# Kernel tuning notes

Measured on AMD Instinct MI355X. Metric: run time of the kernel, lower is better.

The kernel has to match this reference:

```python
import jax, jax.numpy as jnp
import numpy as np

GN_EPS = 1e-5
NN_EPS = 1e-8


def _three_nn_interpolate(xyz1, xyz2, points2):
    # xyz1: (B,N,3), xyz2: (B,M,3), points2: (B,M,C) -> (B,N,C)
    src_sq = jnp.sum(xyz1 ** 2, axis=-1, keepdims=True)          # (B,N,1)
    dst_sq = jnp.sum(xyz2 ** 2, axis=-1)[:, None, :]             # (B,1,M)
    inner = jnp.einsum('bnd,bmd->bnm', xyz1, xyz2)               # (B,N,M)
    dist = src_sq - 2.0 * inner + dst_sq                         # (B,N,M)
    neg_d, idx = jax.lax.top_k(-dist, 3)                         # (B,N,3)
    d = -neg_d
    inv = 1.0 / (d + NN_EPS)
    w = inv / jnp.sum(inv, axis=-1, keepdims=True)               # (B,N,3)
    grouped = jax.vmap(lambda p, i: p[i])(points2, idx)          # (B,N,3,C)
    return jnp.sum(grouped * w[..., None], axis=2)               # (B,N,C)


def _group_norm(x, weight, bias, groups):
    # x: (B,C,N)
    B, C, N = x.shape
    xg = x.reshape(B, groups, C // groups, N)
    mu = jnp.mean(xg, axis=(2, 3), keepdims=True)
    var = jnp.var(xg, axis=(2, 3), keepdims=True)
    xg = (xg - mu) * jax.lax.rsqrt(var + GN_EPS)
    x = xg.reshape(B, C, N)
    return x * weight[None, :, None] + bias[None, :, None]


def setup_inputs() -> dict:
    key = jax.random.key(0)
    ks = jax.random.split(key, 10)
    B, N, M, C1, C2 = 8, 8192, 2048, 128, 256
    mlp = [256, 128]
    in_ch = C1 + C2
    inp = {
        'xyz1': jax.random.normal(ks[0], (B, N, 3), dtype=jnp.float32),
        'xyz2': jax.random.normal(ks[1], (B, M, 3), dtype=jnp.float32),
        'points1': jax.random.normal(ks[2], (B, N, C1), dtype=jnp.float32),
        'points2': jax.random.normal(ks[3], (B, M, C2), dtype=jnp.float32),
        'w0': jax.random.normal(ks[4], (mlp[0], in_ch), dtype=jnp.float32) * (1.0 / np.sqrt(in_ch)),
        'w1': jax.random.normal(ks[5], (mlp[1], mlp[0]), dtype=jnp.float32) * (1.0 / np.sqrt(mlp[0])),
        'gn0_w': jnp.ones((mlp[0],), dtype=jnp.float32),
        'gn0_b': jnp.zeros((mlp[0],), dtype=jnp.float32),
        'gn1_w': jnp.ones((mlp[1],), dtype=jnp.float32),
        'gn1_b': jnp.zeros((mlp[1],), dtype=jnp.float32),
    }
    return inp


def reference(xyz1, xyz2, points1, points2, w0, w1, gn0_w, gn0_b, gn1_w, gn1_b):
    interpolated = _three_nn_interpolate(xyz1, xyz2, points2)    # (B,N,C2)
    feat = jnp.concatenate([points1, interpolated], axis=-1)     # (B,N,C1+C2)
    # conv1d kernel size 1 == pointwise matmul; work in (B,C,N) layout for GN
    h = jnp.einsum('bnc,oc->bon', feat, w0)                      # (B,256,N)
    h = jax.nn.relu(_group_norm(h, gn0_w, gn0_b, groups=min(32, w0.shape[0])))
    h = jnp.einsum('bcn,oc->bon', h, w1)                         # (B,128,N)
    h = jax.nn.relu(_group_norm(h, gn1_w, gn1_b, groups=min(32, w1.shape[0])))
    return jnp.transpose(h, (0, 2, 1))                           # (B,N,128)
```

## Files before the change

### kernel.cpp

```cpp
#include <hip/hip_runtime.h>


#define DEVI __device__ __forceinline__

static constexpr int B  = 8;
static constexpr int N  = 8192;
static constexpr int M  = 2048;
static constexpr int C1 = 128;
static constexpr int C2 = 256;
static constexpr int CIN = C1 + C2;
static constexpr int H0 = 256;
static constexpr int H1 = 128;
static constexpr int BN = B * N;
static constexpr int NSEG = 8;
static constexpr int SEGL = M / NSEG;
static constexpr int SL = 64;

typedef __bf16 bf16x8 __attribute__((ext_vector_type(8)));
typedef float  f32x4  __attribute__((ext_vector_type(4)));
typedef unsigned short ushort8v __attribute__((ext_vector_type(8)));

DEVI float bf2f(unsigned short u) {
    union { unsigned int i; float f; } v; v.i = ((unsigned int)u) << 16; return v.f;
}
DEVI unsigned short f2bf(float f) {
    union { float f; unsigned int i; } v; v.f = f;
    unsigned int x = v.i;
    return (unsigned short)((x + 0x7fffu + ((x >> 16) & 1u)) >> 16);
}
DEVI float ldin(const void* p, size_t i, int bf) {
    return bf ? bf2f(((const unsigned short*)p)[i]) : ((const float*)p)[i];
}
DEVI void ld8(const void* p, size_t i, int bf, float r[8]) {
    if (bf) {
        const ushort8v u = *(const ushort8v*)((const unsigned short*)p + i);
#pragma unroll
        for (int k = 0; k < 8; k++) r[k] = bf2f(u[k]);
    } else {
        const float4 a = *(const float4*)((const float*)p + i);
        const float4 b = *(const float4*)((const float*)p + i + 4);
        r[0] = a.x; r[1] = a.y; r[2] = a.z; r[3] = a.w;
        r[4] = b.x; r[5] = b.y; r[6] = b.z; r[7] = b.w;
    }
}

DEVI void gload16(const void* g, void* l) {
    __builtin_amdgcn_global_load_lds(
        (const __attribute__((address_space(1))) void*)g,
        (__attribute__((address_space(3))) void*)l, 16, 0, 0);
}

__global__ __launch_bounds__(64) void detect_dtype_kernel(const void* __restrict__ xyz1,
                                                          int* __restrict__ flag)
{
    const unsigned short* u = (const unsigned short*)xyz1;
    const int lane = threadIdx.x;
    const float av = fabsf(bf2f(u[2 * lane]));
    const bool in_range = (av >= 1e-4f && av <= 100.0f);
    const unsigned long long m = __ballot(in_range);
    if (lane == 0) flag[0] = (__popcll(m) >= 32) ? 1 : 0;
}

__global__ __launch_bounds__(256) void prep_kernel(
    const void* __restrict__ w0, const void* __restrict__ w1,
    const void* __restrict__ xyz2,
    unsigned short* __restrict__ w0b, unsigned short* __restrict__ w1b,
    float4* __restrict__ c4, const int* __restrict__ flag)
{
    const int bf = flag[0];
    const int n0 = H0 * CIN;
    const int n1 = H1 * H0;
    const int n2 = B * M;
    const int total = n0 + n1 + n2;
    for (int i = blockIdx.x * blockDim.x + threadIdx.x; i < total; i += gridDim.x * blockDim.x) {
        if (i < n0) {
            w0b[i] = bf ? ((const unsigned short*)w0)[i] : f2bf(((const float*)w0)[i]);
        } else if (i < n0 + n1) {
            const int j = i - n0;
            w1b[j] = bf ? ((const unsigned short*)w1)[j] : f2bf(((const float*)w1)[j]);
        } else {
            const int j = i - n0 - n1;
            const float x = ldin(xyz2, (size_t)j * 3 + 0, bf);
            const float y = ldin(xyz2, (size_t)j * 3 + 1, bf);
            const float z = ldin(xyz2, (size_t)j * 3 + 2, bf);
            const float sq = __fadd_rn(__fadd_rn(__fmul_rn(x, x), __fmul_rn(y, y)), __fmul_rn(z, z));
            c4[j] = make_float4(x, y, z, 0.5f * sq);
        }
    }
}

__global__ __launch_bounds__(256) void knn3_split_kernel(
    const void* __restrict__ xyz1, const float4* __restrict__ c4,
    int* __restrict__ ci, const int* __restrict__ flag)
{
    const int bf = flag[0];
    const int tid = threadIdx.x;
    const int gid = blockIdx.x * 256 + tid;
    const int s = blockIdx.y;
    const int b = __builtin_amdgcn_readfirstlane(gid >> 13);

    const float x1 = ldin(xyz1, (size_t)gid * 3 + 0, bf);
    const float y1 = ldin(xyz1, (size_t)gid * 3 + 1, bf);
    const float z1 = ldin(xyz1, (size_t)gid * 3 + 2, bf);

    const float4* __restrict__ cand = c4 + b * M + s * SEGL;
    const int jbase = s * SEGL;

    float b0 = 3.4e38f, b1 = 3.4e38f, b2 = 3.4e38f;
    int   i0 = 0, i1 = 0, i2 = 0;

#pragma unroll 4
    for (int j = 0; j < SEGL; ++j) {
        const float4 p = cand[j];
        const float sc = __builtin_fmaf(-x1, p.x,
                          __builtin_fmaf(-y1, p.y,
                           __builtin_fmaf(-z1, p.z, p.w)));
        const int jn = jbase + j;
        const bool c0 = sc < b0;
        const float t1 = fmaxf(sc, b0);
        b0 = fminf(sc, b0);
        const int  tj1 = c0 ? i0 : jn;
        i0 = c0 ? jn : i0;
        const bool c1 = t1 < b1;
        const float t2 = fmaxf(t1, b1);
        b1 = fminf(t1, b1);
        const int  tj2 = c1 ? i1 : tj1;
        i1 = c1 ? tj1 : i1;
        const bool c2 = t2 < b2;
        b2 = fminf(t2, b2);
        i2 = c2 ? tj2 : i2;
    }

    ci[(size_t)(s * 3 + 0) * BN + gid] = i0;
    ci[(size_t)(s * 3 + 1) * BN + gid] = i1;
    ci[(size_t)(s * 3 + 2) * BN + gid] = i2;
}

__global__ __launch_bounds__(256) void knn3_merge_kernel(
    const void* __restrict__ xyz1, const float4* __restrict__ c4,
    const int* __restrict__ ci,
    int* __restrict__ nn_idx, float* __restrict__ nn_w,
    const int* __restrict__ flag)
{
    const int bf = flag[0];
    const int gid = blockIdx.x * 256 + threadIdx.x;
    const int b = gid >> 13;

    const float x1 = ldin(xyz1, (size_t)gid * 3 + 0, bf);
    const float y1 = ldin(xyz1, (size_t)gid * 3 + 1, bf);
    const float z1 = ldin(xyz1, (size_t)gid * 3 + 2, bf);
    const float sq1 = __fadd_rn(__fadd_rn(__fmul_rn(x1, x1), __fmul_rn(y1, y1)), __fmul_rn(z1, z1));

    float bd0 = 3.4e38f, bd1 = 3.4e38f, bd2 = 3.4e38f;
    int   bi0 = 0x7fffffff, bi1 = 0x7fffffff, bi2 = 0x7fffffff;

#pragma unroll
    for (int k = 0; k < 3 * NSEG; ++k) {
        const int ix = ci[(size_t)k * BN + gid];
        const float4 p = c4[b * M + ix];
        const float inner = __fadd_rn(__fadd_rn(__fmul_rn(x1, p.x), __fmul_rn(y1, p.y)),
                                      __fmul_rn(z1, p.z));
        const float pw2 = p.w + p.w;
        const float d = __fadd_rn(__fsub_rn(sq1, __fmul_rn(2.0f, inner)), pw2);
        const bool lt2 = (d < bd2) || (d == bd2 && ix < bi2);
        if (lt2) {
            const bool lt0 = (d < bd0) || (d == bd0 && ix < bi0);
            const bool lt1 = (d < bd1) || (d == bd1 && ix < bi1);
            if (lt0)      { bd2 = bd1; bi2 = bi1; bd1 = bd0; bi1 = bi0; bd0 = d; bi0 = ix; }
            else if (lt1) { bd2 = bd1; bi2 = bi1; bd1 = d; bi1 = ix; }
            else          { bd2 = d; bi2 = ix; }
        }
    }

    const float v0 = 1.0f / (bd0 + 1e-8f);
    const float v1 = 1.0f / (bd1 + 1e-8f);
    const float v2 = 1.0f / (bd2 + 1e-8f);
    const float s = v0 + v1 + v2;
    nn_idx[gid * 3 + 0] = bi0; nn_idx[gid * 3 + 1] = bi1; nn_idx[gid * 3 + 2] = bi2;
    nn_w[gid * 3 + 0] = v0 / s; nn_w[gid * 3 + 1] = v1 / s; nn_w[gid * 3 + 2] = v2 / s;
}

__global__ __launch_bounds__(256) void interp_concat_kernel(
    const void* __restrict__ p1, const void* __restrict__ p2,
    const int* __restrict__ nn_idx, const float* __restrict__ nn_w,
    unsigned short* __restrict__ feat, const int* __restrict__ flag)
{
    const int bf = flag[0];
    const int total = BN * (CIN / 8);
    for (int idx = blockIdx.x * blockDim.x + threadIdx.x; idx < total; idx += gridDim.x * blockDim.x) {
        const int c8 = idx % 48;
        const int p  = idx / 48;
        const int c  = c8 * 8;
        float r[8];
        if (c < C1) {
            ld8(p1, (size_t)p * C1 + c, bf, r);
        } else {
            const int b  = p >> 13;
            const int c2 = c - C1;
            const int*   id = nn_idx + p * 3;
            const float* wv = nn_w  + p * 3;
            float t0[8], t1[8], t2[8];
            ld8(p2, (size_t)(b * M + id[0]) * C2 + c2, bf, t0);
            ld8(p2, (size_t)(b * M + id[1]) * C2 + c2, bf, t1);
            ld8(p2, (size_t)(b * M + id[2]) * C2 + c2, bf, t2);
            const float w0v = wv[0], w1v = wv[1], w2v = wv[2];
#pragma unroll
            for (int k = 0; k < 8; k++) r[k] = w0v * t0[k] + w1v * t1[k] + w2v * t2[k];
        }
        ushort8v o;
#pragma unroll
        for (int k = 0; k < 8; k++) o[k] = f2bf(r[k]);
        *(ushort8v*)(feat + (size_t)idx * 8) = o;
    }
}

template<int K, int COUT>
__global__ __launch_bounds__(256) void gemm_mfma_kernel(
    const unsigned short* __restrict__ A,
    const unsigned short* __restrict__ W,
    unsigned short* __restrict__ Cmat)
{
    __shared__ __align__(16) char lds[32768];

    const int tid = threadIdx.x;
    const int l   = tid & 63;
    const int w   = tid >> 6;
    const int rowBase = blockIdx.x * 128;
    const int colBase = blockIdx.y * 128;

    const int srow  = l >> 3;
    const int sslot = l & 7;

    f32x4 acc[4][4];
#pragma unroll
    for (int i = 0; i < 4; i++)
#pragma unroll
        for (int j = 0; j < 4; j++) acc[i][j] = (f32x4)0.0f;

    const int wr  = (tid >> 7) & 1;
    const int wc  = (tid >> 6) & 1;
    const int rl  = l & 15;
    const int kq  = l >> 4;
    const int swz = (l & 7) << 4;
    int aoff[4], boff[4];
#pragma unroll
    for (int i = 0; i < 4; i++) {
        aoff[i] = (wr * 64 + i * 16 + rl) * 128;
        boff[i] = 16384 + (wc * 64 + i * 16 + rl) * 128;
    }

    constexpr int NT = K / 64;

#pragma unroll 1
    for (int t = 0; t < NT; ++t) {
        {
            const int k0 = t * 64;
#pragma unroll
            for (int i = 0; i < 4; ++i) {
                const int ch = w * 4 + i;
                const int r  = ch * 8 + srow;
                const int ke = (sslot ^ (r & 7)) << 3;
                gload16(A + ((size_t)(rowBase + r) * K + k0 + ke), lds + ch * 1024);
                gload16(W + ((size_t)(colBase + r) * K + k0 + ke), lds + 16384 + ch * 1024);
            }
        }
        __syncthreads();
#pragma unroll
        for (int ks = 0; ks < 2; ++ks) {
            const int kb = (ks * 64 + kq * 16) ^ swz;
            bf16x8 af[4], bfr[4];
#pragma unroll
            for (int i = 0; i < 4; i++) af[i]  = *(const bf16x8*)(lds + aoff[i] + kb);
#pragma unroll
            for (int j = 0; j < 4; j++) bfr[j] = *(const bf16x8*)(lds + boff[j] + kb);
#pragma unroll
            for (int i = 0; i < 4; i++)
#pragma unroll
                for (int j = 0; j < 4; j++)
                    acc[i][j] = __builtin_amdgcn_mfma_f32_16x16x32_bf16(af[i], bfr[j], acc[i][j], 0, 0, 0);
        }
        __syncthreads();
    }

    const int crow = rowBase + wr * 64 + kq * 4;
    const int ccol = colBase + wc * 64 + rl;
#pragma unroll
    for (int i = 0; i < 4; i++)
#pragma unroll
        for (int j = 0; j < 4; j++)
#pragma unroll
            for (int r = 0; r < 4; r++)
                Cmat[(size_t)(crow + i * 16 + r) * COUT + ccol + j * 16] = f2bf(acc[i][j][r]);
}

__global__ __launch_bounds__(256) void gn_stats_part_kernel(
    const unsigned short* __restrict__ h, float2* __restrict__ part, int C)
{
    const int cpg = C >> 5;
    const int b  = blockIdx.x / SL;
    const int sl = blockIdx.x % SL;
    const int g  = threadIdx.x & 31;
    const int rs = threadIdx.x >> 5;
    const int rows = N / SL;

    float s = 0.f, ss = 0.f;
    for (int n = sl * rows + rs; n < (sl + 1) * rows; n += 8) {
        const unsigned short* row = h + (size_t)(b * N + n) * C + g * cpg;
        for (int c = 0; c < cpg; c += 4) {
            const ushort4 v = *(const ushort4*)(row + c);
            const float f0 = bf2f(v.x), f1 = bf2f(v.y), f2 = bf2f(v.z), f3 = bf2f(v.w);
            s  += f0 + f1 + f2 + f3;
            ss += f0 * f0 + f1 * f1 + f2 * f2 + f3 * f3;
        }
    }
    __shared__ float2 red[256];
    red[threadIdx.x] = make_float2(s, ss);
    __syncthreads();
    if (threadIdx.x < 32) {
        float2 a = red[threadIdx.x];
#pragma unroll
        for (int k = 1; k < 8; k++) {
            const float2 p = red[threadIdx.x + 32 * k];
            a.x += p.x; a.y += p.y;
        }
        part[(size_t)blockIdx.x * 32 + g] = a;
    }
}

__global__ __launch_bounds__(256) void gn_finalize_kernel(
    const float2* __restrict__ part, float2* __restrict__ st, int C)
{
    const int t = threadIdx.x;
    const int b = t >> 5;
    const int g = t & 31;
    const int cpg = C >> 5;
    float s = 0.f, ss = 0.f;
    for (int k = 0; k < SL; k++) {
        const float2 p = part[(size_t)(b * SL + k) * 32 + g];
        s += p.x; ss += p.y;
    }
    const float cnt = (float)N * (float)cpg;
    const float mu  = s / cnt;
    const float var = ss / cnt - mu * mu;
    st[t] = make_float2(mu, rsqrtf(var + 1e-5f));
}

__global__ __launch_bounds__(256) void gn_norm_relu_kernel(
    const unsigned short* __restrict__ h, const float2* __restrict__ st,
    const void* __restrict__ gw, const void* __restrict__ gb,
    void* __restrict__ out, int C, int cpg, int total4,
    const int* __restrict__ flag, int final_out)
{
    const int bf = flag[0];
    const int C4 = C >> 2;
    for (int i4 = blockIdx.x * blockDim.x + threadIdx.x; i4 < total4; i4 += gridDim.x * blockDim.x) {
        const int c = (i4 % C4) * 4;
        const int p = i4 / C4;
        const int b = p >> 13;
        const float2 ms = st[b * (C / cpg) + c / cpg];
        const ushort4 hv = *(const ushort4*)(h + (size_t)i4 * 4);
        float r[4] = { bf2f(hv.x), bf2f(hv.y), bf2f(hv.z), bf2f(hv.w) };
#pragma unroll
        for (int k = 0; k < 4; k++) {
            const float gwv = ldin(gw, c + k, bf);
            const float gbv = ldin(gb, c + k, bf);
            r[k] = fmaxf((r[k] - ms.x) * ms.y * gwv + gbv, 0.f);
        }
        if (!final_out || bf) {
            ushort4 o;
            o.x = f2bf(r[0]); o.y = f2bf(r[1]); o.z = f2bf(r[2]); o.w = f2bf(r[3]);
            *(ushort4*)((unsigned short*)out + (size_t)i4 * 4) = o;
        } else {
            float4 o; o.x = r[0]; o.y = r[1]; o.z = r[2]; o.w = r[3];
            *(float4*)((float*)out + (size_t)i4 * 4) = o;
        }
    }
}

extern "C" void kernel_launch(void* const* d_in, const int* in_sizes, int n_in,
                              void* d_out, int out_size, void* d_ws, size_t ws_size,
                              hipStream_t stream)
{
    const void* xyz1    = d_in[0];
    const void* xyz2    = d_in[1];
    const void* points1 = d_in[2];
    const void* points2 = d_in[3];
    const void* w0      = d_in[4];
    const void* w1      = d_in[5];
    const void* gn0w    = d_in[6];
    const void* gn0b    = d_in[7];
    const void* gn1w    = d_in[8];
    const void* gn1b    = d_in[9];

    char* ws = (char*)d_ws;
    int*            nn_idx = (int*)ws;
    float*          nn_w   = (float*)(ws + 786432);
    unsigned short* feat   = (unsigned short*)(ws + 1572864);
    unsigned short* h0     = (unsigned short*)(ws + 51904512);
    unsigned short* h0n    = feat;
    unsigned short* h1     = h0;
    unsigned short* w0b    = (unsigned short*)(ws + 85458944);
    unsigned short* w1b    = (unsigned short*)(ws + 85655552);
    float2*         st0    = (float2*)(ws + 85721088);
    float2*         st1    = (float2*)(ws + 85723136);
    int*            flag   = (int*)(ws + 85725184);
    float4*         c4     = (float4*)(ws + 85725248);
    int*            ci     = (int*)(ws + 85987392);
    float2*         part   = (float2*)(ws + 92278848);

    detect_dtype_kernel<<<1, 64, 0, stream>>>(xyz1, flag);

    prep_kernel<<<576, 256, 0, stream>>>(w0, w1, xyz2, w0b, w1b, c4, flag);

    {
        dim3 g(BN / 256, NSEG);
        knn3_split_kernel<<<g, 256, 0, stream>>>(xyz1, c4, ci, flag);
    }
    knn3_merge_kernel<<<BN / 256, 256, 0, stream>>>(xyz1, c4, ci, nn_idx, nn_w, flag);

    interp_concat_kernel<<<2048, 256, 0, stream>>>(points1, points2, nn_idx, nn_w, feat, flag);

    {
        dim3 g(BN / 128, H0 / 128);
        gemm_mfma_kernel<CIN, H0><<<g, 256, 0, stream>>>(feat, w0b, h0);
    }

    gn_stats_part_kernel<<<B * SL, 256, 0, stream>>>(h0, part, H0);
    gn_finalize_kernel<<<1, 256, 0, stream>>>(part, st0, H0);
    gn_norm_relu_kernel<<<2048, 256, 0, stream>>>(h0, st0, gn0w, gn0b, (void*)h0n,
                                                  H0, H0 / 32, BN * H0 / 4, flag, 0);

    {
        dim3 g(BN / 128, H1 / 128);
        gemm_mfma_kernel<H0, H1><<<g, 256, 0, stream>>>(h0n, w1b, h1);
    }

    gn_stats_part_kernel<<<B * SL, 256, 0, stream>>>(h1, part, H1);
    gn_finalize_kernel<<<1, 256, 0, stream>>>(part, st1, H1);
    gn_norm_relu_kernel<<<1024, 256, 0, stream>>>(h1, st1, gn1w, gn1b, d_out,
                                                  H1, H1 / 32, BN * H1 / 4, flag, 1);
}
```

Before: 331.7 us.

## Fuse interpolation into GEMM1, GN0 normalize into GEMM2, and GN stats into epilogues

Interpolation and concat now happen while staging the A tile of the first GEMM, so the feat buffer is never written or read back. GroupNorm0 normalize+ReLU is applied while loading the second GEMM's A tile, and GroupNorm statistics are accumulated in the GEMM epilogues with LDS and global atomics. This drops several separate kernels and full-tensor passes. It also splits the KNN scan into two independent interleaved top-3 chains for more ILP. The costs are gather latency inside the GEMM loop, a larger LDS footprint, and float atomics that make the statistics order nondeterministic.

```diff
diff --git a/kernel.cpp b/kernel.cpp
--- a/kernel.cpp
+++ b/kernel.cpp
@@ -14,7 +14,6 @@
 static constexpr int BN = B * N;
 static constexpr int NSEG = 8;
 static constexpr int SEGL = M / NSEG;
-static constexpr int SL = 64;
 
 typedef __bf16 bf16x8 __attribute__((ext_vector_type(8)));
 typedef float  f32x4  __attribute__((ext_vector_type(4)));
@@ -65,26 +64,30 @@
     const void* __restrict__ w0, const void* __restrict__ w1,
     const void* __restrict__ xyz2,
     unsigned short* __restrict__ w0b, unsigned short* __restrict__ w1b,
-    float4* __restrict__ c4, const int* __restrict__ flag)
+    float4* __restrict__ c4, float* __restrict__ partz,
+    const int* __restrict__ flag)
 {
     const int bf = flag[0];
     const int n0 = H0 * CIN;
     const int n1 = H1 * H0;
     const int n2 = B * M;
-    const int total = n0 + n1 + n2;
+    const int n3 = 1024;
+    const int total = n0 + n1 + n2 + n3;
     for (int i = blockIdx.x * blockDim.x + threadIdx.x; i < total; i += gridDim.x * blockDim.x) {
         if (i < n0) {
             w0b[i] = bf ? ((const unsigned short*)w0)[i] : f2bf(((const float*)w0)[i]);
         } else if (i < n0 + n1) {
             const int j = i - n0;
             w1b[j] = bf ? ((const unsigned short*)w1)[j] : f2bf(((const float*)w1)[j]);
-        } else {
+        } else if (i < n0 + n1 + n2) {
             const int j = i - n0 - n1;
             const float x = ldin(xyz2, (size_t)j * 3 + 0, bf);
             const float y = ldin(xyz2, (size_t)j * 3 + 1, bf);
             const float z = ldin(xyz2, (size_t)j * 3 + 2, bf);
             const float sq = __fadd_rn(__fadd_rn(__fmul_rn(x, x), __fmul_rn(y, y)), __fmul_rn(z, z));
             c4[j] = make_float4(x, y, z, 0.5f * sq);
+        } else {
+            partz[i - n0 - n1 - n2] = 0.f;
         }
     }
 }
@@ -105,35 +108,65 @@
 
     const float4* __restrict__ cand = c4 + b * M + s * SEGL;
     const int jbase = s * SEGL;
-
-    float b0 = 3.4e38f, b1 = 3.4e38f, b2 = 3.4e38f;
-    int   i0 = 0, i1 = 0, i2 = 0;
+    constexpr int HALF = SEGL / 2;
+
+    float a0 = 3.4e38f, a1 = 3.4e38f, a2 = 3.4e38f;
+    int   ia0 = 0, ia1 = 0, ia2 = 0;
+    float g0 = 3.4e38f, g1 = 3.4e38f, g2 = 3.4e38f;
+    int   ig0 = 0, ig1 = 0, ig2 = 0;
 
 #pragma unroll 4
-    for (int j = 0; j < SEGL; ++j) {
-        const float4 p = cand[j];
-        const float sc = __builtin_fmaf(-x1, p.x,
-                          __builtin_fmaf(-y1, p.y,
-                           __builtin_fmaf(-z1, p.z, p.w)));
-        const int jn = jbase + j;
-        const bool c0 = sc < b0;
-        const float t1 = fmaxf(sc, b0);
-        b0 = fminf(sc, b0);
-        const int  tj1 = c0 ? i0 : jn;
-        i0 = c0 ? jn : i0;
-        const bool c1 = t1 < b1;
-        const float t2 = fmaxf(t1, b1);
-        b1 = fminf(t1, b1);
-        const int  tj2 = c1 ? i1 : tj1;
-        i1 = c1 ? tj1 : i1;
-        const bool c2 = t2 < b2;
-        b2 = fminf(t2, b2);
-        i2 = c2 ? tj2 : i2;
-    }
-
-    ci[(size_t)(s * 3 + 0) * BN + gid] = i0;
-    ci[(size_t)(s * 3 + 1) * BN + gid] = i1;
-    ci[(size_t)(s * 3 + 2) * BN + gid] = i2;
+    for (int j = 0; j < HALF; ++j) {
+        const float4 pA = cand[j];
+        const float4 pB = cand[j + HALF];
+        const float sA = __builtin_fmaf(-x1, pA.x,
+                          __builtin_fmaf(-y1, pA.y,
+                           __builtin_fmaf(-z1, pA.z, pA.w)));
+        const float sB = __builtin_fmaf(-x1, pB.x,
+                          __builtin_fmaf(-y1, pB.y,
+                           __builtin_fmaf(-z1, pB.z, pB.w)));
+        {
+            const int jn = jbase + j;
+            const bool c0 = sA < a0;
+            const float t1 = fmaxf(sA, a0); a0 = fminf(sA, a0);
+            const int  tj1 = c0 ? ia0 : jn; ia0 = c0 ? jn : ia0;
+            const bool c1 = t1 < a1;
+            const float t2 = fmaxf(t1, a1); a1 = fminf(t1, a1);
+            const int  tj2 = c1 ? ia1 : tj1; ia1 = c1 ? tj1 : ia1;
+            const bool c2 = t2 < a2;
+            a2 = fminf(t2, a2); ia2 = c2 ? tj2 : ia2;
+        }
+        {
+            const int jn = jbase + HALF + j;
+            const bool c0 = sB < g0;
+            const float t1 = fmaxf(sB, g0); g0 = fminf(sB, g0);
+            const int  tj1 = c0 ? ig0 : jn; ig0 = c0 ? jn : ig0;
+            const bool c1 = t1 < g1;
+            const float t2 = fmaxf(t1, g1); g1 = fminf(t1, g1);
+            const int  tj2 = c1 ? ig1 : tj1; ig1 = c1 ? tj1 : ig1;
+            const bool c2 = t2 < g2;
+            g2 = fminf(t2, g2); ig2 = c2 ? tj2 : ig2;
+        }
+    }
+
+    float mv[3] = { g0, g1, g2 };
+    int   mi[3] = { ig0, ig1, ig2 };
+#pragma unroll
+    for (int k = 0; k < 3; ++k) {
+        const float sv = mv[k]; const int jn = mi[k];
+        const bool c0 = sv < a0;
+        const float t1 = fmaxf(sv, a0); a0 = fminf(sv, a0);
+        const int  tj1 = c0 ? ia0 : jn; ia0 = c0 ? jn : ia0;
+        const bool c1 = t1 < a1;
+        const float t2 = fmaxf(t1, a1); a1 = fminf(t1, a1);
+        const int  tj2 = c1 ? ia1 : tj1; ia1 = c1 ? tj1 : ia1;
+        const bool c2 = t2 < a2;
+        a2 = fminf(t2, a2); ia2 = c2 ? tj2 : ia2;
+    }
+
+    ci[(size_t)(s * 3 + 0) * BN + gid] = ia0;
+    ci[(size_t)(s * 3 + 1) * BN + gid] = ia1;
+    ci[(size_t)(s * 3 + 2) * BN + gid] = ia2;
 }
 
 __global__ __launch_bounds__(256) void knn3_merge_kernel(
@@ -180,53 +213,161 @@
     nn_w[gid * 3 + 0] = v0 / s; nn_w[gid * 3 + 1] = v1 / s; nn_w[gid * 3 + 2] = v2 / s;
 }
 
-__global__ __launch_bounds__(256) void interp_concat_kernel(
+__global__ __launch_bounds__(256, 2) void gemm1_kernel(
     const void* __restrict__ p1, const void* __restrict__ p2,
     const int* __restrict__ nn_idx, const float* __restrict__ nn_w,
-    unsigned short* __restrict__ feat, const int* __restrict__ flag)
-{
+    const unsigned short* __restrict__ W,
+    unsigned short* __restrict__ h0, float2* __restrict__ part,
+    const int* __restrict__ flag)
+{
+    constexpr int K = CIN;
+    constexpr int COUT = H0;
+    __shared__ __align__(16) char lds[49152];
+
     const int bf = flag[0];
-    const int total = BN * (CIN / 8);
-    for (int idx = blockIdx.x * blockDim.x + threadIdx.x; idx < total; idx += gridDim.x * blockDim.x) {
-        const int c8 = idx % 48;
-        const int p  = idx / 48;
-        const int c  = c8 * 8;
-        float r[8];
-        if (c < C1) {
-            ld8(p1, (size_t)p * C1 + c, bf, r);
-        } else {
-            const int b  = p >> 13;
-            const int c2 = c - C1;
-            const int*   id = nn_idx + p * 3;
-            const float* wv = nn_w  + p * 3;
-            float t0[8], t1[8], t2[8];
-            ld8(p2, (size_t)(b * M + id[0]) * C2 + c2, bf, t0);
-            ld8(p2, (size_t)(b * M + id[1]) * C2 + c2, bf, t1);
-            ld8(p2, (size_t)(b * M + id[2]) * C2 + c2, bf, t2);
-            const float w0v = wv[0], w1v = wv[1], w2v = wv[2];
-#pragma unroll
-            for (int k = 0; k < 8; k++) r[k] = w0v * t0[k] + w1v * t1[k] + w2v * t2[k];
-        }
-        ushort8v o;
-#pragma unroll
-        for (int k = 0; k < 8; k++) o[k] = f2bf(r[k]);
-        *(ushort8v*)(feat + (size_t)idx * 8) = o;
-    }
-}
-
-template<int K, int COUT>
-__global__ __launch_bounds__(256) void gemm_mfma_kernel(
-    const unsigned short* __restrict__ A,
-    const unsigned short* __restrict__ W,
-    unsigned short* __restrict__ Cmat)
-{
-    __shared__ __align__(16) char lds[32768];
-
     const int tid = threadIdx.x;
     const int l   = tid & 63;
     const int w   = tid >> 6;
     const int rowBase = blockIdx.x * 128;
-    const int colBase = blockIdx.y * 128;
+    const int b = rowBase >> 13;
+
+    const int srow  = l >> 3;
+    const int sslot = l & 7;
+
+    int arow[4]; int aidx[4][3]; float aw[4][3];
+#pragma unroll
+    for (int i = 0; i < 4; i++) {
+        const int r = (w * 4 + i) * 8 + srow;
+        arow[i] = r;
+        const int p = rowBase + r;
+#pragma unroll
+        for (int k = 0; k < 3; k++) {
+            aidx[i][k] = nn_idx[p * 3 + k];
+            aw[i][k]   = nn_w[p * 3 + k];
+        }
+    }
+
+    f32x4 acc[4][8];
+#pragma unroll
+    for (int i = 0; i < 4; i++)
+#pragma unroll
+        for (int j = 0; j < 8; j++) acc[i][j] = (f32x4)0.0f;
+
+    const int wr  = (tid >> 7) & 1;
+    const int wc  = (tid >> 6) & 1;
+    const int rl  = l & 15;
+    const int kq  = l >> 4;
+    const int swz = (l & 7) << 4;
+    int aoff[4], boff[8];
+#pragma unroll
+    for (int i = 0; i < 4; i++) aoff[i] = (wr * 64 + i * 16 + rl) * 128;
+#pragma unroll
+    for (int j = 0; j < 8; j++) boff[j] = 16384 + (wc * 128 + j * 16 + rl) * 128;
+
+    constexpr int NT = K / 64;
+
+#pragma unroll 1
+    for (int t = 0; t < NT; ++t) {
+        const int k0 = t * 64;
+#pragma unroll
+        for (int i = 0; i < 8; ++i) {
+            const int cb = w * 8 + i;
+            const int r  = cb * 8 + srow;
+            const int ke = (sslot ^ (r & 7)) << 3;
+            gload16(W + ((size_t)r * K + k0 + ke), lds + 16384 + cb * 1024);
+        }
+#pragma unroll
+        for (int i = 0; i < 4; ++i) {
+            const int r = arow[i];
+            const int kslot = sslot ^ (r & 7);
+            const int c = k0 + (kslot << 3);
+            float v[8];
+            if (k0 < C1) {
+                ld8(p1, (size_t)(rowBase + r) * C1 + c, bf, v);
+            } else {
+                const int c2 = c - C1;
+                float t0[8], t1[8], t2[8];
+                ld8(p2, (size_t)(b * M + aidx[i][0]) * C2 + c2, bf, t0);
+                ld8(p2, (size_t)(b * M + aidx[i][1]) * C2 + c2, bf, t1);
+                ld8(p2, (size_t)(b * M + aidx[i][2]) * C2 + c2, bf, t2);
+                const float w0v = aw[i][0], w1v = aw[i][1], w2v = aw[i][2];
+#pragma unroll
+                for (int k = 0; k < 8; k++) v[k] = w0v * t0[k] + w1v * t1[k] + w2v * t2[k];
+            }
+            ushort8v o;
+#pragma unroll
+            for (int k = 0; k < 8; k++) o[k] = f2bf(v[k]);
+            *(ushort8v*)(lds + r * 128 + (sslot << 4)) = o;
+        }
+        __syncthreads();
+#pragma unroll
+        for (int ks = 0; ks < 2; ++ks) {
+            const int kb = (ks * 64 + kq * 16) ^ swz;
+            bf16x8 af[4], bfr[8];
+#pragma unroll
+            for (int i = 0; i < 4; i++) af[i]  = *(const bf16x8*)(lds + aoff[i] + kb);
+#pragma unroll
+            for (int j = 0; j < 8; j++) bfr[j] = *(const bf16x8*)(lds + boff[j] + kb);
+#pragma unroll
+            for (int i = 0; i < 4; i++)
+#pragma unroll
+                for (int j = 0; j < 8; j++)
+                    acc[i][j] = __builtin_amdgcn_mfma_f32_16x16x32_bf16(af[i], bfr[j], acc[i][j], 0, 0, 0);
+        }
+        __syncthreads();
+    }
+
+    const int crow = rowBase + wr * 64 + kq * 4;
+    const int ccol = wc * 128 + rl;
+    float gsum[8], gss[8];
+#pragma unroll
+    for (int j = 0; j < 8; j++) {
+        float s = 0.f, ss = 0.f;
+#pragma unroll
+        for (int i = 0; i < 4; i++)
+#pragma unroll
+            for (int r = 0; r < 4; r++) {
+                const unsigned short hb = f2bf(acc[i][j][r]);
+                h0[(size_t)(crow + i * 16 + r) * COUT + ccol + j * 16] = hb;
+                const float x = bf2f(hb);
+                s += x; ss += x * x;
+            }
+        gsum[j] = s; gss[j] = ss;
+    }
+    __syncthreads();
+    float2* sred = (float2*)lds;
+    if (tid < 32) sred[tid] = make_float2(0.f, 0.f);
+    __syncthreads();
+#pragma unroll
+    for (int j = 0; j < 8; j++) {
+        const int g = wc * 16 + j * 2 + (rl >> 3);
+        atomicAdd(&sred[g].x, gsum[j]);
+        atomicAdd(&sred[g].y, gss[j]);
+    }
+    __syncthreads();
+    if (tid < 32) {
+        atomicAdd(&part[b * 32 + tid].x, sred[tid].x);
+        atomicAdd(&part[b * 32 + tid].y, sred[tid].y);
+    }
+}
+
+__global__ __launch_bounds__(256) void gemm2_kernel(
+    const unsigned short* __restrict__ h0, const float2* __restrict__ st0,
+    const void* __restrict__ gw, const void* __restrict__ gb,
+    const unsigned short* __restrict__ W,
+    unsigned short* __restrict__ h1, float2* __restrict__ part,
+    const int* __restrict__ flag)
+{
+    constexpr int K = H0;
+    constexpr int COUT = H1;
+    __shared__ __align__(16) char lds[32768];
+
+    const int bf = flag[0];
+    const int tid = threadIdx.x;
+    const int l   = tid & 63;
+    const int w   = tid >> 6;
+    const int rowBase = blockIdx.x * 128;
+    const int b = rowBase >> 13;
 
     const int srow  = l >> 3;
     const int sslot = l & 7;
@@ -253,16 +394,31 @@
 
 #pragma unroll 1
     for (int t = 0; t < NT; ++t) {
-        {
-            const int k0 = t * 64;
-#pragma unroll
-            for (int i = 0; i < 4; ++i) {
-                const int ch = w * 4 + i;
-                const int r  = ch * 8 + srow;
-                const int ke = (sslot ^ (r & 7)) << 3;
-                gload16(A + ((size_t)(rowBase + r) * K + k0 + ke), lds + ch * 1024);
-                gload16(W + ((size_t)(colBase + r) * K + k0 + ke), lds + 16384 + ch * 1024);
+        const int k0 = t * 64;
+#pragma unroll
+        for (int i = 0; i < 4; ++i) {
+            const int cb = w * 4 + i;
+            const int r  = cb * 8 + srow;
+            const int ke = (sslot ^ (r & 7)) << 3;
+            gload16(W + ((size_t)r * K + k0 + ke), lds + 16384 + cb * 1024);
+        }
+#pragma unroll
+        for (int i = 0; i < 4; ++i) {
+            const int r = (w * 4 + i) * 8 + srow;
+            const int kslot = sslot ^ (r & 7);
+            const int c = k0 + (kslot << 3);
+            const float2 ms = st0[b * 32 + (c >> 3)];
+            float gwv[8], gbv[8];
+            ld8(gw, c, bf, gwv);
+            ld8(gb, c, bf, gbv);
+            const ushort8v hv = *(const ushort8v*)(h0 + (size_t)(rowBase + r) * H0 + c);
+            ushort8v o;
+#pragma unroll
+            for (int k = 0; k < 8; k++) {
+                const float x = bf2f(hv[k]);
+                o[k] = f2bf(fmaxf((x - ms.x) * ms.y * gwv[k] + gbv[k], 0.f));
             }
+            *(ushort8v*)(lds + r * 128 + (sslot << 4)) = o;
         }
         __syncthreads();
 #pragma unroll
@@ -283,65 +439,46 @@
     }
 
     const int crow = rowBase + wr * 64 + kq * 4;
-    const int ccol = colBase + wc * 64 + rl;
-#pragma unroll
-    for (int i = 0; i < 4; i++)
-#pragma unroll
-        for (int j = 0; j < 4; j++)
-#pragma unroll
-            for (int r = 0; r < 4; r++)
-                Cmat[(size_t)(crow + i * 16 + r) * COUT + ccol + j * 16] = f2bf(acc[i][j][r]);
-}
-
-__global__ __launch_bounds__(256) void gn_stats_part_kernel(
-    const unsigned short* __restrict__ h, float2* __restrict__ part, int C)
-{
-    const int cpg = C >> 5;
-    const int b  = blockIdx.x / SL;
-    const int sl = blockIdx.x % SL;
-    const int g  = threadIdx.x & 31;
-    const int rs = threadIdx.x >> 5;
-    const int rows = N / SL;
-
-    float s = 0.f, ss = 0.f;
-    for (int n = sl * rows + rs; n < (sl + 1) * rows; n += 8) {
-        const unsigned short* row = h + (size_t)(b * N + n) * C + g * cpg;
-        for (int c = 0; c < cpg; c += 4) {
-            const ushort4 v = *(const ushort4*)(row + c);
-            const float f0 = bf2f(v.x), f1 = bf2f(v.y), f2 = bf2f(v.z), f3 = bf2f(v.w);
-            s  += f0 + f1 + f2 + f3;
-            ss += f0 * f0 + f1 * f1 + f2 * f2 + f3 * f3;
-        }
-    }
-    __shared__ float2 red[256];
-    red[threadIdx.x] = make_float2(s, ss);
+    const int ccol = wc * 64 + rl;
+    float gsum[4], gss[4];
+#pragma unroll
+    for (int j = 0; j < 4; j++) {
+        float s = 0.f, ss = 0.f;
+#pragma unroll
+        for (int i = 0; i < 4; i++)
+#pragma unroll
+            for (int r = 0; r < 4; r++) {
+                const unsigned short hb = f2bf(acc[i][j][r]);
+                h1[(size_t)(crow + i * 16 + r) * COUT + ccol + j * 16] = hb;
+                const float x = bf2f(hb);
+                s += x; ss += x * x;
+            }
+        gsum[j] = s; gss[j] = ss;
+    }
     __syncthreads();
-    if (threadIdx.x < 32) {
-        float2 a = red[threadIdx.x];
-#pragma unroll
-        for (int k = 1; k < 8; k++) {
-            const float2 p = red[threadIdx.x + 32 * k];
-            a.x += p.x; a.y += p.y;
-        }
-        part[(size_t)blockIdx.x * 32 + g] = a;
+    float2* sred = (float2*)lds;
+    if (tid < 32) sred[tid] = make_float2(0.f, 0.f);
+    __syncthreads();
+#pragma unroll
+    for (int j = 0; j < 4; j++) {
+        const int g = wc * 16 + j * 4 + (rl >> 2);
+        atomicAdd(&sred[g].x, gsum[j]);
+        atomicAdd(&sred[g].y, gss[j]);
+    }
+    __syncthreads();
+    if (tid < 32) {
+        atomicAdd(&part[b * 32 + tid].x, sred[tid].x);
+        atomicAdd(&part[b * 32 + tid].y, sred[tid].y);
     }
 }
 
 __global__ __launch_bounds__(256) void gn_finalize_kernel(
-    const float2* __restrict__ part, float2* __restrict__ st, int C)
+    const float2* __restrict__ part, float2* __restrict__ st, float cnt)
 {
     const int t = threadIdx.x;
-    const int b = t >> 5;
-    const int g = t & 31;
-    const int cpg = C >> 5;
-    float s = 0.f, ss = 0.f;
-    for (int k = 0; k < SL; k++) {
-        const float2 p = part[(size_t)(b * SL + k) * 32 + g];
-        s += p.x; ss += p.y;
-    }
-    const float cnt = (float)N * (float)cpg;
-    const float mu  = s / cnt;
-    const float var = ss / cnt - mu * mu;
+    const float2 p = part[t];
+    const float mu  = p.x / cnt;
+    const float var = p.y / cnt - mu * mu;
     st[t] = make_float2(mu, rsqrtf(var + 1e-5f));
 }
 
@@ -349,7 +486,7 @@
     const unsigned short* __restrict__ h, const float2* __restrict__ st,
     const void* __restrict__ gw, const void* __restrict__ gb,
     void* __restrict__ out, int C, int cpg, int total4,
-    const int* __restrict__ flag, int final_out)
+    const int* __restrict__ flag)
 {
     const int bf = flag[0];
     const int C4 = C >> 2;
@@ -366,7 +503,7 @@
             const float gbv = ldin(gb, c + k, bf);
             r[k] = fmaxf((r[k] - ms.x) * ms.y * gwv + gbv, 0.f);
         }
-        if (!final_out || bf) {
+        if (bf) {
             ushort4 o;
             o.x = f2bf(r[0]); o.y = f2bf(r[1]); o.z = f2bf(r[2]); o.w = f2bf(r[3]);
             *(ushort4*)((unsigned short*)out + (size_t)i4 * 4) = o;
@@ -395,22 +532,21 @@
     char* ws = (char*)d_ws;
     int*            nn_idx = (int*)ws;
     float*          nn_w   = (float*)(ws + 786432);
-    unsigned short* feat   = (unsigned short*)(ws + 1572864);
-    unsigned short* h0     = (unsigned short*)(ws + 51904512);
-    unsigned short* h0n    = feat;
-    unsigned short* h1     = h0;
-    unsigned short* w0b    = (unsigned short*)(ws + 85458944);
-    unsigned short* w1b    = (unsigned short*)(ws + 85655552);
-    float2*         st0    = (float2*)(ws + 85721088);
-    float2*         st1    = (float2*)(ws + 85723136);
-    int*            flag   = (int*)(ws + 85725184);
-    float4*         c4     = (float4*)(ws + 85725248);
-    int*            ci     = (int*)(ws + 85987392);
-    float2*         part   = (float2*)(ws + 92278848);
+    unsigned short* h0     = (unsigned short*)(ws + 1572864);
+    unsigned short* h1     = (unsigned short*)(ws + 35127296);
+    unsigned short* w0b    = (unsigned short*)(ws + 51904512);
+    unsigned short* w1b    = (unsigned short*)(ws + 52101120);
+    float2*         st0    = (float2*)(ws + 52166656);
+    float2*         st1    = (float2*)(ws + 52168704);
+    int*            flag   = (int*)(ws + 52170752);
+    float4*         c4     = (float4*)(ws + 52170816);
+    int*            ci     = (int*)(ws + 52432960);
+    float2*         part0  = (float2*)(ws + 58724416);
+    float2*         part1  = (float2*)(ws + 58726464);
 
     detect_dtype_kernel<<<1, 64, 0, stream>>>(xyz1, flag);
 
-    prep_kernel<<<576, 256, 0, stream>>>(w0, w1, xyz2, w0b, w1b, c4, flag);
+    prep_kernel<<<576, 256, 0, stream>>>(w0, w1, xyz2, w0b, w1b, c4, (float*)part0, flag);
 
     {
         dim3 g(BN / 256, NSEG);
@@ -418,25 +554,13 @@
     }
     knn3_merge_kernel<<<BN / 256, 256, 0, stream>>>(xyz1, c4, ci, nn_idx, nn_w, flag);
 
-    interp_concat_kernel<<<2048, 256, 0, stream>>>(points1, points2, nn_idx, nn_w, feat, flag);
-
-    {
-        dim3 g(BN / 128, H0 / 128);
-        gemm_mfma_kernel<CIN, H0><<<g, 256, 0, stream>>>(feat, w0b, h0);
-    }
-
-    gn_stats_part_kernel<<<B * SL, 256, 0, stream>>>(h0, part, H0);
-    gn_finalize_kernel<<<1, 256, 0, stream>>>(part, st0, H0);
-    gn_norm_relu_kernel<<<2048, 256, 0, stream>>>(h0, st0, gn0w, gn0b, (void*)h0n,
-                                                  H0, H0 / 32, BN * H0 / 4, flag, 0);
-
-    {
-        dim3 g(BN / 128, H1 / 128);
-        gemm_mfma_kernel<H0, H1><<<g, 256, 0, stream>>>(h0n, w1b, h1);
-    }
-
-    gn_stats_part_kernel<<<B * SL, 256, 0, stream>>>(h1, part, H1);
-    gn_finalize_kernel<<<1, 256, 0, stream>>>(part, st1, H1);
+    gemm1_kernel<<<BN / 128, 256, 0, stream>>>(points1, points2, nn_idx, nn_w,
+                                               w0b, h0, part0, flag);
+    gn_finalize_kernel<<<1, 256, 0, stream>>>(part0, st0, (float)N * (H0 / 32));
+
+    gemm2_kernel<<<BN / 128, 256, 0, stream>>>(h0, st0, gn0w, gn0b, w1b, h1, part1, flag);
+    gn_finalize_kernel<<<1, 256, 0, stream>>>(part1, st1, (float)N * (H1 / 32));
+
     gn_norm_relu_kernel<<<1024, 256, 0, stream>>>(h1, st1, gn1w, gn1b, d_out,
-                                                  H1, H1 / 32, BN * H1 / 4, flag, 1);
-}
+                                                  H1, H1 / 32, BN * H1 / 4, flag);
+}
```

After: 353.7 us. +6.6%, slower.
